# Optimization experiments

Hardware: AMD Instinct MI355X
Metric: run time of the kernel (lower is better)

## Reference

```python
import jax, jax.numpy as jnp
import numpy as np

BETA = 1.0
G_MAX = 2.0
DECAY_RATE = 0.05
RECOVERY_RATE = 0.1
U_MIN, U_MAX = 0.01, 0.2


def setup_inputs() -> dict:
    key = jax.random.key(0)
    k1, _ = jax.random.split(key)
    B = 1048576
    u_initial = jax.random.uniform(k1, (B,), dtype=jnp.float32)  # unemployment in [0,1)
    u_trigger = jnp.float32(0.06)  # learnable threshold parameter
    return {"u_initial": u_initial, "u_trigger": u_trigger, "steps": 256}


def reference(u_initial, u_trigger, steps):
    def step(u, _):
        g = G_MAX * jax.nn.sigmoid(BETA * (u - u_trigger))
        u_next = jnp.clip(u + (DECAY_RATE - RECOVERY_RATE * g), U_MIN, U_MAX)
        return u_next, (u_next, g)

    _, (u_hist, g_hist) = jax.lax.scan(step, u_initial, None, length=steps)
    # u_hist, g_hist: [steps, B]
    return u_hist, g_hist
```

## Files before the change

### kernel.cpp

```cpp
#include <hip/hip_runtime.h>


#define VEC 4
#define UNROLL 8

__global__ __launch_bounds__(256) void stimulus_kernel(
    const float* __restrict__ u_init,
    const float* __restrict__ ut_p,
    float* __restrict__ u_hist,
    float* __restrict__ g_hist,
    int B, int steps)
{
    const int tid = blockIdx.x * blockDim.x + threadIdx.x;
    const size_t base = (size_t)tid * VEC;
    if (base >= (size_t)B) return;

    const float ut = ut_p[0];

    float4 in = *(const float4*)(u_init + base);
    float u[VEC] = {in.x, in.y, in.z, in.w};

    float* up = u_hist + base;
    float* gp = g_hist + base;

    float4 ubuf[UNROLL], gbuf[UNROLL];

    for (int t0 = 0; t0 < steps; t0 += UNROLL) {
        #pragma unroll
        for (int s = 0; s < UNROLL; ++s) {
            float g[VEC];
            #pragma unroll
            for (int j = 0; j < VEC; ++j) {
                float e = __expf(ut - u[j]);
                float gg = 2.0f * __builtin_amdgcn_rcpf(1.0f + e);
                float un = u[j] + (0.05f - 0.1f * gg);
                un = fminf(fmaxf(un, 0.01f), 0.2f);
                u[j] = un;
                g[j] = gg;
            }
            ubuf[s] = make_float4(u[0], u[1], u[2], u[3]);
            gbuf[s] = make_float4(g[0], g[1], g[2], g[3]);
        }
        #pragma unroll
        for (int s = 0; s < UNROLL; ++s) {
            *(float4*)up = ubuf[s];
            *(float4*)gp = gbuf[s];
            up += B;
            gp += B;
        }
    }
}

extern "C" void kernel_launch(void* const* d_in, const int* in_sizes, int n_in,
                              void* d_out, int out_size, void* d_ws, size_t ws_size,
                              hipStream_t stream) {
    const float* u_init = (const float*)d_in[0];
    const float* ut     = (const float*)d_in[1];
    const int B = in_sizes[0];
    const int steps = out_size / (2 * B);

    float* u_hist = (float*)d_out;
    float* g_hist = u_hist + (size_t)steps * (size_t)B;

    const int threads = (B + VEC - 1) / VEC;
    const int block = 256;
    const int grid = (threads + block - 1) / block;
    hipLaunchKernelGGL(stimulus_kernel, dim3(grid), dim3(block), 0, stream,
                       u_init, ut, u_hist, g_hist, B, steps);
}
```

Baseline: 2.195 ms.

## Split time steps across two blocks with recomputed prefix to double parallelism

Each column block is now launched twice. One copy writes the first half of the time steps. The other copy silently recomputes the first half of the recurrence and then writes the second half. This doubles the number of wavefronts so the GPU gets more memory-level parallelism for the store-bound output. The price is redundant transcendental math. The 8-step store batching is also removed, and the kernel assumes an even step count.

Measured after the change: 2.195 ms. Within noise of the previous version (+0.0%).

```diff
diff --git a/kernel.cpp b/kernel.cpp
--- a/kernel.cpp
+++ b/kernel.cpp
@@ -2,7 +2,7 @@
 
 
 #define VEC 4
-#define UNROLL 8
+#define TSPLIT 2
 
 __global__ __launch_bounds__(256) void stimulus_kernel(
     const float* __restrict__ u_init,
@@ -11,43 +11,48 @@
     float* __restrict__ g_hist,
     int B, int steps)
 {
-    const int tid = blockIdx.x * blockDim.x + threadIdx.x;
+    const int half = blockIdx.x & (TSPLIT - 1);
+    const int cb   = blockIdx.x >> 1;
+    const int tid  = cb * blockDim.x + threadIdx.x;
     const size_t base = (size_t)tid * VEC;
     if (base >= (size_t)B) return;
 
     const float ut = ut_p[0];
+    const int half_steps = steps / TSPLIT;
+    const int t_begin = half * half_steps;
+    const int t_end   = t_begin + half_steps;
 
     float4 in = *(const float4*)(u_init + base);
     float u[VEC] = {in.x, in.y, in.z, in.w};
 
-    float* up = u_hist + base;
-    float* gp = g_hist + base;
+    for (int t = 0; t < t_begin; ++t) {
+        #pragma unroll
+        for (int j = 0; j < VEC; ++j) {
+            float e = __expf(ut - u[j]);
+            float gg = 2.0f * __builtin_amdgcn_rcpf(1.0f + e);
+            float un = u[j] + (0.05f - 0.1f * gg);
+            u[j] = fminf(fmaxf(un, 0.01f), 0.2f);
+        }
+    }
 
-    float4 ubuf[UNROLL], gbuf[UNROLL];
+    float* up = u_hist + (size_t)t_begin * B + base;
+    float* gp = g_hist + (size_t)t_begin * B + base;
 
-    for (int t0 = 0; t0 < steps; t0 += UNROLL) {
+    for (int t = t_begin; t < t_end; ++t) {
+        float g[VEC];
         #pragma unroll
-        for (int s = 0; s < UNROLL; ++s) {
-            float g[VEC];
-            #pragma unroll
-            for (int j = 0; j < VEC; ++j) {
-                float e = __expf(ut - u[j]);
-                float gg = 2.0f * __builtin_amdgcn_rcpf(1.0f + e);
-                float un = u[j] + (0.05f - 0.1f * gg);
-                un = fminf(fmaxf(un, 0.01f), 0.2f);
-                u[j] = un;
-                g[j] = gg;
-            }
-            ubuf[s] = make_float4(u[0], u[1], u[2], u[3]);
-            gbuf[s] = make_float4(g[0], g[1], g[2], g[3]);
+        for (int j = 0; j < VEC; ++j) {
+            float e = __expf(ut - u[j]);
+            float gg = 2.0f * __builtin_amdgcn_rcpf(1.0f + e);
+            float un = u[j] + (0.05f - 0.1f * gg);
+            un = fminf(fmaxf(un, 0.01f), 0.2f);
+            u[j] = un;
+            g[j] = gg;
         }
-        #pragma unroll
-        for (int s = 0; s < UNROLL; ++s) {
-            *(float4*)up = ubuf[s];
-            *(float4*)gp = gbuf[s];
-            up += B;
-            gp += B;
-        }
+        *(float4*)up = make_float4(u[0], u[1], u[2], u[3]);
+        *(float4*)gp = make_float4(g[0], g[1], g[2], g[3]);
+        up += B;
+        gp += B;
     }
 }
 
@@ -64,7 +69,7 @@
 
     const int threads = (B + VEC - 1) / VEC;
     const int block = 256;
-    const int grid = (threads + block - 1) / block;
+    const int grid = ((threads + block - 1) / block) * TSPLIT;
     hipLaunchKernelGGL(stimulus_kernel, dim3(grid), dim3(block), 0, stream,
                        u_init, ut, u_hist, g_hist, B, steps);
 }
```
